# Optimization experiments

Hardware: AMD Instinct MI355X
Metric: run time of the kernel (lower is better)

## Reference

```python
import jax, jax.numpy as jnp
import numpy as np

NATOMS_PER_TYPE = (128, 128)  # natom = 256 split across 2 atom types
EI_MEAN = (-3.37, -4.50)
NFEAT, H1, H2 = 42, 50, 50


def _fcnet(x, W0, b0, W1, b1, W2, b2):
    # x: [B, n_type, F]; tanh MLP, linear output head -> per-atom energy [B, n_type, 1]
    h0 = jnp.tanh(x @ W0 + b0)
    h1 = jnp.tanh(h0 @ W1 + b1)
    return h1 @ W2 + b2


def _ei_all(image, params):
    # per-atom-type MLP over contiguous atom slices, concat -> Ei [B, natom, 1]
    outs, off = [], 0
    for t, n in enumerate(NATOMS_PER_TYPE):
        outs.append(_fcnet(image[:, off:off + n], *params[t]))
        off += n
    return jnp.concatenate(outs, axis=1)


def setup_inputs() -> dict:
    key = jax.random.key(0)
    ks = jax.random.split(key, 16)
    B, natom, nn = 32, 256, 100
    inp = {
        'image': jax.random.normal(ks[0], (B, natom, NFEAT), dtype=jnp.float32),
        'dfeat': jax.random.normal(ks[1], (B, natom, nn, NFEAT, 3), dtype=jnp.float32),
        'neighbor': jax.random.randint(ks[2], (B, natom, nn), 0, natom + 1, dtype=jnp.int64),
    }
    def xav(k, fan_in, fan_out):
        s = np.sqrt(6.0 / (fan_in + fan_out))
        return jax.random.uniform(k, (fan_in, fan_out), jnp.float32, -s, s)
    for t in range(2):
        kk = jax.random.split(ks[3 + t], 3)
        inp[f'W0_t{t}'] = xav(kk[0], NFEAT, H1)
        inp[f'b0_t{t}'] = jnp.zeros((H1,), jnp.float32)
        inp[f'W1_t{t}'] = xav(kk[1], H1, H2)
        inp[f'b1_t{t}'] = jnp.zeros((H2,), jnp.float32)
        inp[f'W2_t{t}'] = xav(kk[2], H2, 1)
        inp[f'b2_t{t}'] = jnp.array([EI_MEAN[t]], jnp.float32)
    return inp


def reference(image, dfeat, neighbor,
              W0_t0, b0_t0, W1_t0, b1_t0, W2_t0, b2_t0,
              W0_t1, b0_t1, W1_t1, b1_t1, W2_t1, b2_t1):
    params = ((W0_t0, b0_t0, W1_t0, b1_t0, W2_t0, b2_t0),
              (W0_t1, b0_t1, W1_t1, b1_t1, W2_t1, b2_t1))
    Ei = _ei_all(image, params)          # [B, natom, 1]
    Etot = Ei.sum(axis=1)                # [B, 1]
    # test_grad = d(sum Ei)/d(image), matches torch.autograd.grad in the original
    test_grad = jax.grad(lambda img: _ei_all(img, params).sum())(image)  # [B, natom, F]
    B, natom, F = image.shape
    # fortran-style: index 0 -> zero row (no neighbor), 1..natom -> atoms
    dE_pad = jnp.concatenate([jnp.zeros((B, 1, F), image.dtype), test_grad], axis=1)
    nbr_dE = dE_pad[jnp.arange(B)[:, None, None], neighbor]  # [B, natom, nn, F]
    Force = jnp.einsum('bnkf,bnkfd->bnd', nbr_dE, dfeat)     # [B, natom, 3]
    return (Etot, Ei, Force)
```

## Files before the change

### kernel.cpp

```cpp
#include <hip/hip_runtime.h>
#include <cstdint>

#define BB 32
#define NATOM 256
#define NN 100
#define NF 42
#define HH 50
#define PADROWS 257
#define DE_STRIDE (PADROWS * NF)

__device__ __forceinline__ float fast_tanh(float x) {
    const float e = __expf(2.0f * x);
    return 1.0f - 2.0f / (e + 1.0f);
}

__global__ __launch_bounds__(128) void mlp_fwd_bwd(
    const float* __restrict__ image,
    const float* __restrict__ W0a, const float* __restrict__ b0a,
    const float* __restrict__ W1a, const float* __restrict__ b1a,
    const float* __restrict__ W2a, const float* __restrict__ b2a,
    const float* __restrict__ W0b, const float* __restrict__ b0b,
    const float* __restrict__ W1b, const float* __restrict__ b1b,
    const float* __restrict__ W2b, const float* __restrict__ b2b,
    float* __restrict__ outEtot,
    float* __restrict__ outEi,
    float* __restrict__ dEp)
{
    __shared__ float W0s[NF * HH];
    __shared__ float W1s[HH * HH];
    __shared__ float W2s[HH], b0s[HH], b1s[HH];
    __shared__ float b2s;
    __shared__ float red[128];

    const int blk  = blockIdx.x;
    const int b    = blk >> 1;
    const int half = blk & 1;
    const int tid  = threadIdx.x;

    const float* W0 = half ? W0b : W0a;
    const float* b0 = half ? b0b : b0a;
    const float* W1 = half ? W1b : W1a;
    const float* b1 = half ? b1b : b1a;
    const float* W2 = half ? W2b : W2a;
    const float* b2 = half ? b2b : b2a;

    for (int i = tid; i < NF * HH; i += 128) W0s[i] = W0[i];
    for (int i = tid; i < HH * HH; i += 128) W1s[i] = W1[i];
    if (tid < HH) { W2s[tid] = W2[tid]; b0s[tid] = b0[tid]; b1s[tid] = b1[tid]; }
    if (tid == 0) b2s = b2[0];

    if (half == 0 && tid < NF) dEp[(size_t)b * DE_STRIDE + tid] = 0.0f;
    __syncthreads();

    const int n = half * 128 + tid;
    const int g = b * NATOM + n;

    float x[NF];
    {
        const float2* xp = (const float2*)(image + (size_t)g * NF);
        #pragma unroll
        for (int f = 0; f < NF / 2; ++f) {
            const float2 v = xp[f];
            x[2 * f] = v.x;
            x[2 * f + 1] = v.y;
        }
    }

    float h0[HH], h1[HH];

    for (int j = 0; j < HH; j += 2) {
        float s0 = b0s[j], s1 = b0s[j + 1];
        #pragma unroll
        for (int f = 0; f < NF; ++f) {
            const float xf = x[f];
            s0 += xf * W0s[f * HH + j];
            s1 += xf * W0s[f * HH + j + 1];
        }
        h0[j] = fast_tanh(s0);
        h0[j + 1] = fast_tanh(s1);
    }

    for (int j = 0; j < HH; j += 2) {
        float s0 = b1s[j], s1 = b1s[j + 1];
        #pragma unroll
        for (int i = 0; i < HH; ++i) {
            const float hi = h0[i];
            s0 += hi * W1s[i * HH + j];
            s1 += hi * W1s[i * HH + j + 1];
        }
        h1[j] = fast_tanh(s0);
        h1[j + 1] = fast_tanh(s1);
    }

    float Ei0 = 0.0f, Ei1 = 0.0f;
    for (int j = 0; j < HH; j += 2) {
        Ei0 += h1[j] * W2s[j];
        Ei1 += h1[j + 1] * W2s[j + 1];
    }
    const float Ei = Ei0 + Ei1 + b2s;
    outEi[g] = Ei;

    red[tid] = Ei;
    __syncthreads();
    for (int o = 64; o > 0; o >>= 1) {
        if (tid < o) red[tid] += red[tid + o];
        __syncthreads();
    }
    if (tid == 0) atomicAdd(&outEtot[b], red[0]);

    #pragma unroll
    for (int j = 0; j < HH; ++j) {
        const float t = h1[j];
        h1[j] = W2s[j] * (1.0f - t * t);
    }
    for (int i = 0; i < HH; i += 2) {
        float s0 = 0.0f, s1 = 0.0f;
        #pragma unroll
        for (int j = 0; j < HH; ++j) {
            const float gj = h1[j];
            s0 += gj * W1s[i * HH + j];
            s1 += gj * W1s[(i + 1) * HH + j];
        }
        const float t0 = h0[i], t1 = h0[i + 1];
        h0[i] = s0 * (1.0f - t0 * t0);
        h0[i + 1] = s1 * (1.0f - t1 * t1);
    }
    float2* dxp = (float2*)(dEp + (size_t)b * DE_STRIDE + (size_t)(1 + n) * NF);
    for (int f = 0; f < NF; f += 2) {
        float s0 = 0.0f, s1 = 0.0f;
        #pragma unroll
        for (int i = 0; i < HH; ++i) {
            const float gi = h0[i];
            s0 += gi * W0s[f * HH + i];
            s1 += gi * W0s[(f + 1) * HH + i];
        }
        dxp[f >> 1] = make_float2(s0, s1);
    }
}

__global__ __launch_bounds__(256) void force_kernel(
    const float* __restrict__ dfeat,
    const int* __restrict__ neighbor,
    const float* __restrict__ dEp,
    float* __restrict__ outForce)
{
    __shared__ int   nbr_s[NN];
    __shared__ float dE_s[NN * NF];
    __shared__ float part[4][3];

    const int bn  = blockIdx.x;
    const int b   = bn >> 8;
    const int tid = threadIdx.x;
    const int w   = tid >> 6;
    const int l   = tid & 63;

    const int start = (w < 2) ? 13 * w : 26 + 12 * (w - 2);
    const int cnt   = (w < 2) ? 13 : 12;

    float4 v[13];
    const float4* df4 = (const float4*)dfeat + (size_t)bn * 3150;
    if (l < 63) {
        #pragma unroll
        for (int i = 0; i < 13; ++i) {
            int p = start + i;
            if (p > 49) p = 49;
            v[i] = df4[p * 63 + l];
        }
        if (w >= 2) v[12] = make_float4(0.0f, 0.0f, 0.0f, 0.0f);
    }

    if (tid < NN) nbr_s[tid] = neighbor[(size_t)bn * NN + tid];
    __syncthreads();
    {
        const float* dEb = dEp + (size_t)b * DE_STRIDE;
        for (int q = tid; q < NN * NF; q += 256) {
            const int k = q / NF;
            const int f = q - k * NF;
            dE_s[q] = dEb[nbr_s[k] * NF + f];
        }
    }
    __syncthreads();

    float acc0 = 0.0f, acc1 = 0.0f, acc2 = 0.0f, acc3 = 0.0f;
    int d0 = 0, d1 = 0, d2 = 0, d3 = 0;
    float s0 = 0.0f, s1 = 0.0f, s2 = 0.0f;
    if (l < 63) {
        int off0, off1, off2, off3;
        const int r = 4 * l;
        #define DECOMP(c, OFF, DD) { int rc = r + (c); int ko = (rc >= 126) ? 1 : 0; \
            int rr = rc - 126 * ko; int f = rr / 3; (DD) = rr - 3 * f; (OFF) = ko * NF + f; }
        DECOMP(0, off0, d0) DECOMP(1, off1, d1) DECOMP(2, off2, d2) DECOMP(3, off3, d3)
        #undef DECOMP

        #pragma unroll
        for (int i = 0; i < 13; ++i) {
            int p = start + i;
            if (p > 49) p = 49;
            const float* base = dE_s + 84 * p;
            acc0 += v[i].x * base[off0];
            acc1 += v[i].y * base[off1];
            acc2 += v[i].z * base[off2];
            acc3 += v[i].w * base[off3];
        }

        s0 = (d0 == 0 ? acc0 : 0.0f) + (d1 == 0 ? acc1 : 0.0f) +
             (d2 == 0 ? acc2 : 0.0f) + (d3 == 0 ? acc3 : 0.0f);
        s1 = (d0 == 1 ? acc0 : 0.0f) + (d1 == 1 ? acc1 : 0.0f) +
             (d2 == 1 ? acc2 : 0.0f) + (d3 == 1 ? acc3 : 0.0f);
        s2 = (d0 == 2 ? acc0 : 0.0f) + (d1 == 2 ? acc1 : 0.0f) +
             (d2 == 2 ? acc2 : 0.0f) + (d3 == 2 ? acc3 : 0.0f);
    }

    #pragma unroll
    for (int m = 32; m > 0; m >>= 1) {
        s0 += __shfl_xor(s0, m);
        s1 += __shfl_xor(s1, m);
        s2 += __shfl_xor(s2, m);
    }
    if (l == 0) { part[w][0] = s0; part[w][1] = s1; part[w][2] = s2; }
    __syncthreads();
    if (tid < 3)
        outForce[(size_t)bn * 3 + tid] =
            part[0][tid] + part[1][tid] + part[2][tid] + part[3][tid];
}

extern "C" void kernel_launch(void* const* d_in, const int* in_sizes, int n_in,
                              void* d_out, int out_size, void* d_ws, size_t ws_size,
                              hipStream_t stream) {
    const float* image    = (const float*)d_in[0];
    const float* dfeat    = (const float*)d_in[1];
    const int*   neighbor = (const int*)d_in[2];
    const float* W0_t0 = (const float*)d_in[3];
    const float* b0_t0 = (const float*)d_in[4];
    const float* W1_t0 = (const float*)d_in[5];
    const float* b1_t0 = (const float*)d_in[6];
    const float* W2_t0 = (const float*)d_in[7];
    const float* b2_t0 = (const float*)d_in[8];
    const float* W0_t1 = (const float*)d_in[9];
    const float* b0_t1 = (const float*)d_in[10];
    const float* W1_t1 = (const float*)d_in[11];
    const float* b1_t1 = (const float*)d_in[12];
    const float* W2_t1 = (const float*)d_in[13];
    const float* b2_t1 = (const float*)d_in[14];

    float* outEtot  = (float*)d_out;
    float* outEi    = outEtot + BB;
    float* outForce = outEi + BB * NATOM;
    float* dEp      = (float*)d_ws;

    hipMemsetAsync(d_out, 0, BB * sizeof(float), stream);

    mlp_fwd_bwd<<<64, 128, 0, stream>>>(
        image,
        W0_t0, b0_t0, W1_t0, b1_t0, W2_t0, b2_t0,
        W0_t1, b0_t1, W1_t1, b1_t1, W2_t1, b2_t1,
        outEtot, outEi, dEp);

    force_kernel<<<BB * NATOM, 256, 0, stream>>>(dfeat, neighbor, dEp, outForce);
}
```

Baseline: 625.4 us.

## Split MLP blocks to one wavefront, drop memset and atomics, vectorize dE gather

The MLP kernel now runs 128 blocks of 64 threads instead of 64 blocks of 128, which doubles the number of blocks working on this small serial stage. Per-block energy sums use a wavefront shuffle reduction and are written to a partial buffer rather than atomically added. The force kernel then finalizes Etot, which removes the memset launch. The dE neighbor gather into shared memory now uses float2 loads. Each block still loads the full weight set into shared memory, so total weight traffic doubles.

```diff
diff --git a/kernel.cpp b/kernel.cpp
--- a/kernel.cpp
+++ b/kernel.cpp
@@ -14,7 +14,7 @@
     return 1.0f - 2.0f / (e + 1.0f);
 }
 
-__global__ __launch_bounds__(128) void mlp_fwd_bwd(
+__global__ __launch_bounds__(64) void mlp_fwd_bwd(
     const float* __restrict__ image,
     const float* __restrict__ W0a, const float* __restrict__ b0a,
     const float* __restrict__ W1a, const float* __restrict__ b1a,
@@ -22,20 +22,20 @@
     const float* __restrict__ W0b, const float* __restrict__ b0b,
     const float* __restrict__ W1b, const float* __restrict__ b1b,
     const float* __restrict__ W2b, const float* __restrict__ b2b,
-    float* __restrict__ outEtot,
     float* __restrict__ outEi,
-    float* __restrict__ dEp)
+    float* __restrict__ dEp,
+    float* __restrict__ Epart)
 {
     __shared__ float W0s[NF * HH];
     __shared__ float W1s[HH * HH];
     __shared__ float W2s[HH], b0s[HH], b1s[HH];
     __shared__ float b2s;
-    __shared__ float red[128];
-
-    const int blk  = blockIdx.x;
-    const int b    = blk >> 1;
-    const int half = blk & 1;
-    const int tid  = threadIdx.x;
+
+    const int blk = blockIdx.x;
+    const int b   = blk >> 2;
+    const int q   = blk & 3;
+    const int half = q >> 1;
+    const int tid = threadIdx.x;
 
     const float* W0 = half ? W0b : W0a;
     const float* b0 = half ? b0b : b0a;
@@ -44,15 +44,15 @@
     const float* W2 = half ? W2b : W2a;
     const float* b2 = half ? b2b : b2a;
 
-    for (int i = tid; i < NF * HH; i += 128) W0s[i] = W0[i];
-    for (int i = tid; i < HH * HH; i += 128) W1s[i] = W1[i];
+    for (int i = tid; i < NF * HH; i += 64) W0s[i] = W0[i];
+    for (int i = tid; i < HH * HH; i += 64) W1s[i] = W1[i];
     if (tid < HH) { W2s[tid] = W2[tid]; b0s[tid] = b0[tid]; b1s[tid] = b1[tid]; }
     if (tid == 0) b2s = b2[0];
 
-    if (half == 0 && tid < NF) dEp[(size_t)b * DE_STRIDE + tid] = 0.0f;
-    __syncthreads();
-
-    const int n = half * 128 + tid;
+    if (q == 0 && tid < NF) dEp[(size_t)b * DE_STRIDE + tid] = 0.0f;
+    __syncthreads();
+
+    const int n = q * 64 + tid;
     const int g = b * NATOM + n;
 
     float x[NF];
@@ -100,13 +100,10 @@
     const float Ei = Ei0 + Ei1 + b2s;
     outEi[g] = Ei;
 
-    red[tid] = Ei;
-    __syncthreads();
-    for (int o = 64; o > 0; o >>= 1) {
-        if (tid < o) red[tid] += red[tid + o];
-        __syncthreads();
-    }
-    if (tid == 0) atomicAdd(&outEtot[b], red[0]);
+    float s = Ei;
+    #pragma unroll
+    for (int m = 32; m > 0; m >>= 1) s += __shfl_xor(s, m);
+    if (tid == 0) Epart[b * 4 + q] = s;
 
     #pragma unroll
     for (int j = 0; j < HH; ++j) {
@@ -142,6 +139,8 @@
     const float* __restrict__ dfeat,
     const int* __restrict__ neighbor,
     const float* __restrict__ dEp,
+    const float* __restrict__ Epart,
+    float* __restrict__ outEtot,
     float* __restrict__ outForce)
 {
     __shared__ int   nbr_s[NN];
@@ -155,7 +154,6 @@
     const int l   = tid & 63;
 
     const int start = (w < 2) ? 13 * w : 26 + 12 * (w - 2);
-    const int cnt   = (w < 2) ? 13 : 12;
 
     float4 v[13];
     const float4* df4 = (const float4*)dfeat + (size_t)bn * 3150;
@@ -172,19 +170,20 @@
     if (tid < NN) nbr_s[tid] = neighbor[(size_t)bn * NN + tid];
     __syncthreads();
     {
-        const float* dEb = dEp + (size_t)b * DE_STRIDE;
-        for (int q = tid; q < NN * NF; q += 256) {
-            const int k = q / NF;
-            const int f = q - k * NF;
-            dE_s[q] = dEb[nbr_s[k] * NF + f];
-        }
-    }
-    __syncthreads();
-
-    float acc0 = 0.0f, acc1 = 0.0f, acc2 = 0.0f, acc3 = 0.0f;
+        const float2* dEb2 = (const float2*)(dEp + (size_t)b * DE_STRIDE);
+        float2* dEs2 = (float2*)dE_s;
+        for (int q = tid; q < NN * (NF / 2); q += 256) {
+            const int k = q / (NF / 2);
+            const int f2 = q - k * (NF / 2);
+            dEs2[q] = dEb2[nbr_s[k] * (NF / 2) + f2];
+        }
+    }
+    __syncthreads();
+
     int d0 = 0, d1 = 0, d2 = 0, d3 = 0;
     float s0 = 0.0f, s1 = 0.0f, s2 = 0.0f;
     if (l < 63) {
+        float acc0 = 0.0f, acc1 = 0.0f, acc2 = 0.0f, acc3 = 0.0f;
         int off0, off1, off2, off3;
         const int r = 4 * l;
         #define DECOMP(c, OFF, DD) { int rc = r + (c); int ko = (rc >= 126) ? 1 : 0; \
@@ -222,6 +221,10 @@
     if (tid < 3)
         outForce[(size_t)bn * 3 + tid] =
             part[0][tid] + part[1][tid] + part[2][tid] + part[3][tid];
+
+    if ((bn & 255) == 0 && tid == 3)
+        outEtot[b] = Epart[b * 4] + Epart[b * 4 + 1] +
+                     Epart[b * 4 + 2] + Epart[b * 4 + 3];
 }
 
 extern "C" void kernel_launch(void* const* d_in, const int* in_sizes, int n_in,
@@ -247,14 +250,14 @@
     float* outEi    = outEtot + BB;
     float* outForce = outEi + BB * NATOM;
     float* dEp      = (float*)d_ws;
-
-    hipMemsetAsync(d_out, 0, BB * sizeof(float), stream);
-
-    mlp_fwd_bwd<<<64, 128, 0, stream>>>(
+    float* Epart    = dEp + BB * DE_STRIDE;
+
+    mlp_fwd_bwd<<<128, 64, 0, stream>>>(
         image,
         W0_t0, b0_t0, W1_t0, b1_t0, W2_t0, b2_t0,
         W0_t1, b0_t1, W1_t1, b1_t1, W2_t1, b2_t1,
-        outEtot, outEi, dEp);
-
-    force_kernel<<<BB * NATOM, 256, 0, stream>>>(dfeat, neighbor, dEp, outForce);
-}
+        outEi, dEp, Epart);
+
+    force_kernel<<<BB * NATOM, 256, 0, stream>>>(dfeat, neighbor, dEp, Epart,
+                                                 outEtot, outForce);
+}
```

Measured after the change: 621.5 us. Within noise of the previous version (-0.6%).
